# Performance work log

Hardware: AMD Instinct MI355X
Metric: run time of the kernel (lower is better)

## Reference

```python
import math
import jax, jax.numpy as jnp
import numpy as np

EPS = 1e-08
W_BLK = 256  # covers max window w = exp(log 255) + 1 = 256


def _l2norm(x):
    n = jnp.linalg.norm(x, axis=-1, keepdims=True)
    return x / jnp.maximum(n, EPS)


def setup_inputs() -> dict:
    key = jax.random.key(0)
    ks = jax.random.split(key, 7)
    B, T, Dm, H = 2, 4096, 1024, 16
    scale = 1.0 / math.sqrt(Dm)
    return {
        "query": jax.random.normal(ks[0], (B, T, Dm), jnp.float32),
        "key": jax.random.normal(ks[1], (B, T, Dm), jnp.float32),
        "value": jax.random.normal(ks[2], (B, T, Dm), jnp.float32),
        "Wq": jax.random.normal(ks[3], (Dm, Dm), jnp.float32) * scale,
        "Wk": jax.random.normal(ks[4], (Dm, Dm), jnp.float32) * scale,
        "Wv": jax.random.normal(ks[5], (Dm, Dm), jnp.float32) * scale,
        "Wo": jax.random.normal(ks[6], (Dm, Dm), jnp.float32) * scale,
        "s_v": jnp.linspace(0.0, math.log(255.0), H).astype(jnp.float32),
        "s_r": jnp.zeros((H,), jnp.float32),
    }


def _screening_forward(query, key, value, Wq, Wk, Wv, Wo, s_v, s_r):
    B, T, Dm = query.shape
    H = s_v.shape[0]
    D = Dm // H

    def proj(x, Wm):  # nn.Linear (no bias): x @ W^T, then split heads -> [B,H,T,D]
        return (x @ Wm.T).reshape(B, T, H, D).transpose(0, 2, 1, 3)

    q = _l2norm(proj(query, Wq))
    k = _l2norm(proj(key, Wk))
    v = _l2norm(proj(value, Wv))

    w = jnp.exp(s_v) + 1.0  # [H] window widths, <= 256
    r = jnp.exp(s_r) + 1.0  # [H] screening sharpness

    Wb = W_BLK
    nb = T // Wb
    qb = q.reshape(B, H, nb, Wb, D)
    kb = k.reshape(B, H, nb, Wb, D)
    vb = v.reshape(B, H, nb, Wb, D)
    # each query block attends to its own block + previous block (window <= Wb)
    kprev = jnp.pad(kb, ((0, 0), (0, 0), (1, 0), (0, 0), (0, 0)))[:, :, :nb]
    vprev = jnp.pad(vb, ((0, 0), (0, 0), (1, 0), (0, 0), (0, 0)))[:, :, :nb]
    kc = jnp.concatenate([kprev, kb], axis=3)  # [B,H,nb,2W,D]
    vc = jnp.concatenate([vprev, vb], axis=3)

    sim = jnp.einsum('bhnid,bhnjd->bhnij', qb, kc)  # [B,H,nb,W,2W]

    ii = jnp.arange(Wb)[:, None]
    jj = jnp.arange(2 * Wb)[None, :]
    rel = (jj - (Wb + ii)).astype(jnp.float32)  # [W,2W] relative offset j-i
    wb_ = w[:, None, None]  # [H,1,1]
    cos_m = 0.5 * (jnp.cos(jnp.pi * rel[None] / wb_) + 1.0)  # [H,W,2W]
    in_w = (rel[None] > -wb_) & (rel[None] <= 0.0)  # causal window
    softmask = cos_m * in_w.astype(sim.dtype)  # [H,W,2W]
    # block 0 has no previous block: first Wb key slots invalid there
    blk_valid = ((jnp.arange(nb)[:, None] > 0) | (jnp.arange(2 * Wb)[None, :] >= Wb))

    alpha = jax.nn.relu(1.0 - r[None, :, None, None, None] * (1.0 - sim)) ** 2
    alpha = alpha * softmask[None, :, None] * blk_valid.astype(sim.dtype)[None, None, :, None, :]

    out = jnp.einsum('bhnij,bhnjd->bhnid', alpha, vc).reshape(B, H, T, D)
    # TanhNorm: smoothly bound vector magnitude (tanh of the L2 norm)
    n = jnp.linalg.norm(out, axis=-1, keepdims=True)
    out = out * jnp.tanh(n) / (n + EPS)
    out = out.transpose(0, 2, 1, 3).reshape(B, T, Dm)
    return out @ Wo.T


def reference(query, key, value, Wq, Wk, Wv, Wo, s_v, s_r):
    return _screening_forward(query, key, value, Wq, Wk, Wv, Wo, s_v, s_r)
```

## Files before the change

kernel.cpp:

```cpp
#include <hip/hip_runtime.h>
#include <math.h>

#ifndef M_PI
#define M_PI 3.14159265358979323846
#endif

typedef short bf16x8 __attribute__((ext_vector_type(8)));
typedef _Float16 f16x8 __attribute__((ext_vector_type(8)));
typedef float f32x4 __attribute__((ext_vector_type(4)));

union FragU { uint4 u; bf16x8 f; };
union F16U { uint4 u; f16x8 f; _Float16 h[8]; };

typedef const __attribute__((address_space(1))) void GVoid;
typedef __attribute__((address_space(3))) void LVoid;

__device__ __forceinline__ unsigned rn_hi(float x) {
    unsigned u = __float_as_uint(x);
    unsigned r = u + 0x7FFFu + ((u >> 16) & 1u);
    return r & 0xFFFF0000u;
}

__global__ void mask_tab_kernel(const float* __restrict__ s_v, float* __restrict__ tab) {
    int h = blockIdx.x;
    int idx = threadIdx.x;
    float w = expf(s_v[h]) + 1.0f;
    float rel = (float)(idx - 255);
    float val = 0.0f;
    if (rel > -w) {
        val = 0.5f * (cosf((float)M_PI * rel / w) + 1.0f);
    }
    tab[h * 256 + idx] = val;
}

__global__ __launch_bounds__(256) void split_tiles(
        const float* __restrict__ in0, const float* __restrict__ in1,
        const float* __restrict__ in2, char* __restrict__ out0,
        unsigned long long ostride) {
    const float* in = (blockIdx.y == 0) ? in0 : (blockIdx.y == 1) ? in1 : in2;
    char* outp = out0 + (size_t)blockIdx.y * ostride;
    const int tile = blockIdx.x;
    const int kt = tile & 31;
    const int rb = tile >> 5;
    const int tid = threadIdx.x;
    const int row = tid >> 1;
    const int kc = (tid & 1) * 16;

    const float* src = in + ((size_t)(rb * 128 + row)) * 1024 + kt * 32 + kc;
    f32x4 x0 = *(const f32x4*)src;
    f32x4 x1 = *(const f32x4*)(src + 4);
    f32x4 x2 = *(const f32x4*)(src + 8);
    f32x4 x3 = *(const f32x4*)(src + 12);
    float xs[16] = {x0[0], x0[1], x0[2], x0[3], x1[0], x1[1], x1[2], x1[3],
                    x2[0], x2[1], x2[2], x2[3], x3[0], x3[1], x3[2], x3[3]};
    F16U h0, h1, l0, l1;
#pragma unroll
    for (int e = 0; e < 8; e++) {
        _Float16 h = (_Float16)xs[e];
        h0.h[e] = h;
        l0.h[e] = (_Float16)(xs[e] - (float)h);
        _Float16 h2 = (_Float16)xs[8 + e];
        h1.h[e] = h2;
        l1.h[e] = (_Float16)(xs[8 + e] - (float)h2);
    }
    char* tb = outp + (size_t)tile * 16384 + row * 128;
    const int swz = (row & 7) << 4;
    *(uint4*)(tb + ((kc * 2) ^ swz))           = h0.u;
    *(uint4*)(tb + ((kc * 2 + 16) ^ swz))      = h1.u;
    *(uint4*)(tb + ((64 + kc * 2) ^ swz))      = l0.u;
    *(uint4*)(tb + ((64 + kc * 2 + 16) ^ swz)) = l1.u;
}

__device__ __forceinline__ void cvt_split16(const f32x4* a, F16U& h0, F16U& h1,
                                            F16U& l0, F16U& l1) {
    float xs[16] = {a[0][0], a[0][1], a[0][2], a[0][3],
                    a[1][0], a[1][1], a[1][2], a[1][3],
                    a[2][0], a[2][1], a[2][2], a[2][3],
                    a[3][0], a[3][1], a[3][2], a[3][3]};
#pragma unroll
    for (int e = 0; e < 8; e++) {
        _Float16 h = (_Float16)xs[e];
        h0.h[e] = h;
        l0.h[e] = (_Float16)(xs[e] - (float)h);
        _Float16 h2 = (_Float16)xs[8 + e];
        h1.h[e] = h2;
        l1.h[e] = (_Float16)(xs[8 + e] - (float)h2);
    }
}

template <int PERM>
__global__ __launch_bounds__(256, 2) void gemm_ws(
        const float* __restrict__ A0, const float* __restrict__ A1,
        const float* __restrict__ A2,
        const char* __restrict__ Bsp, unsigned long long Bstride,
        float* __restrict__ C0, float* __restrict__ C1, float* __restrict__ C2) {
    __shared__ __align__(16) char Abuf[16384];
    __shared__ __align__(16) char Bbuf[65536];

    const int tid = threadIdx.x;
    const int bid = blockIdx.x;
    const int o = bid >> 8;
    const int x = bid & 255;
    const int xcd = x & 7;
    const int idx = x >> 3;
    const int rp = xcd * 8 + (idx >> 2);
    const int cp = idx & 3;
    const int brow = rp * 128;
    const int bcol = cp * 256;

    const float* A = (o == 0) ? A0 : (o == 1) ? A1 : A2;
    float* C = (o == 0) ? C0 : (o == 1) ? C1 : C2;
    const char* Bt = Bsp + (size_t)o * Bstride;

    const int lane = tid & 63;
    const int wid = tid >> 6;
    const int wr = wid >> 1;
    const int wc = wid & 1;
    const int l15 = lane & 15;
    const int g = lane >> 4;

    const int srow = tid >> 1;
    const int skc2 = (tid & 1) * 32;
    const float* aptr = A + (size_t)(brow + srow) * 1024 + (tid & 1) * 16;
    const int aswz = (srow & 7) << 4;
    char* awr = Abuf + srow * 128;

    const char* bsrc = Bt + ((size_t)(cp * 2 + (wid >> 1)) * 32) * 16384
                       + (wid & 1) * 8192;

    const int rswz = (l15 & 7) << 4;

    f32x4 acc[4][8];
#pragma unroll
    for (int a = 0; a < 4; a++)
#pragma unroll
        for (int b = 0; b < 8; b++) acc[a][b] = (f32x4)(0.0f);

    f32x4 areg[4];
#pragma unroll
    for (int m = 0; m < 4; m++) areg[m] = *(const f32x4*)(aptr + m * 4);
    F16U Sh0, Sh1, Sl0, Sl1;
    cvt_split16(areg, Sh0, Sh1, Sl0, Sl1);
#pragma unroll
    for (int i = 0; i < 8; i++)
        __builtin_amdgcn_global_load_lds(
            (GVoid*)(bsrc + i * 1024 + lane * 16),
            (LVoid*)(Bbuf + wid * 8192 + i * 1024), 16, 0, 0);

#pragma unroll 1
    for (int kt = 0; kt < 32; kt++) {
        __syncthreads();
        *(uint4*)(awr + ((skc2) ^ aswz))      = Sh0.u;
        *(uint4*)(awr + ((skc2 + 16) ^ aswz)) = Sh1.u;
        *(uint4*)(awr + ((skc2 + 64) ^ aswz)) = Sl0.u;
        *(uint4*)(awr + ((skc2 + 80) ^ aswz)) = Sl1.u;
        __syncthreads();

        if (kt + 1 < 32) {
            const char* bs = bsrc + (size_t)(kt + 1) * 16384;
            const int nxt = ((kt + 1) & 1) * 32768;
#pragma unroll
            for (int i = 0; i < 8; i++)
                __builtin_amdgcn_global_load_lds(
                    (GVoid*)(bs + i * 1024 + lane * 16),
                    (LVoid*)(Bbuf + nxt + wid * 8192 + i * 1024), 16, 0, 0);
#pragma unroll
            for (int m = 0; m < 4; m++)
                areg[m] = *(const f32x4*)(aptr + (kt + 1) * 32 + m * 4);
        }

        const char* bb = Bbuf + (kt & 1) * 32768 + wc * 16384;
        f16x8 ah[4], al[4];
#pragma unroll
        for (int fr = 0; fr < 4; fr++) {
            const int ro = (wr * 64 + fr * 16 + l15) * 128;
            ah[fr] = *(const f16x8*)(Abuf + ro + ((g * 16) ^ rswz));
            al[fr] = *(const f16x8*)(Abuf + ro + ((g * 16) ^ rswz ^ 64));
        }
#pragma unroll
        for (int fc = 0; fc < 8; fc++) {
            const int ro = (fc * 16 + l15) * 128;
            f16x8 bh = *(const f16x8*)(bb + ro + ((g * 16) ^ rswz));
            f16x8 bl = *(const f16x8*)(bb + ro + ((g * 16) ^ rswz ^ 64));
#pragma unroll
            for (int fr = 0; fr < 4; fr++) {
                acc[fr][fc] = __builtin_amdgcn_mfma_f32_16x16x32_f16(
                    ah[fr], bh, acc[fr][fc], 0, 0, 0);
                acc[fr][fc] = __builtin_amdgcn_mfma_f32_16x16x32_f16(
                    ah[fr], bl, acc[fr][fc], 0, 0, 0);
                acc[fr][fc] = __builtin_amdgcn_mfma_f32_16x16x32_f16(
                    al[fr], bh, acc[fr][fc], 0, 0, 0);
            }
        }
        if (kt + 1 < 32) cvt_split16(areg, Sh0, Sh1, Sl0, Sl1);
    }

    if (PERM == 1) {
#pragma unroll
        for (int fr = 0; fr < 4; fr++) {
#pragma unroll
            for (int r = 0; r < 4; r++) {
                float p0 = 0.0f, p1 = 0.0f;
#pragma unroll
                for (int fc = 0; fc < 4; fc++) {
                    p0 = fmaf(acc[fr][fc][r], acc[fr][fc][r], p0);
                    p1 = fmaf(acc[fr][fc + 4][r], acc[fr][fc + 4][r], p1);
                }
                p0 += __shfl_xor(p0, 1);  p1 += __shfl_xor(p1, 1);
                p0 += __shfl_xor(p0, 2);  p1 += __shfl_xor(p1, 2);
                p0 += __shfl_xor(p0, 4);  p1 += __shfl_xor(p1, 4);
                p0 += __shfl_xor(p0, 8);  p1 += __shfl_xor(p1, 8);
                float i0 = 1.0f / fmaxf(sqrtf(p0), 1e-8f);
                float i1 = 1.0f / fmaxf(sqrtf(p1), 1e-8f);
#pragma unroll
                for (int fc = 0; fc < 4; fc++) {
                    acc[fr][fc][r] *= i0;
                    acc[fr][fc + 4][r] *= i1;
                }
            }
        }
    }

    const int rsub = g * 4;
#pragma unroll
    for (int fr = 0; fr < 4; fr++) {
#pragma unroll
        for (int fc = 0; fc < 8; fc++) {
            f32x4 v = acc[fr][fc];
            const int i0 = brow + wr * 64 + fr * 16 + rsub;
            const int j0 = bcol + wc * 128 + fc * 16;
            if (PERM == 0) {
#pragma unroll
                for (int r = 0; r < 4; r++)
                    C[(size_t)(i0 + r) * 1024 + j0 + l15] = v[r];
            } else {
                const int h = j0 >> 6;
                const int d = (j0 & 63) + l15;
#pragma unroll
                for (int r = 0; r < 4; r++) {
                    const int i = i0 + r;
                    const int b = i >> 12;
                    const int t2 = i & 4095;
                    C[(((size_t)(b * 16 + h) * 4096 + t2) * 64 + d)] = v[r];
                }
            }
        }
    }
}

__global__ __launch_bounds__(256, 3) void attn_kernel(
        const float* __restrict__ q, const float* __restrict__ k,
        const float* __restrict__ v, const float* __restrict__ s_v,
        const float* __restrict__ s_r, const float* __restrict__ mask_tab,
        float* __restrict__ out) {
    __shared__ unsigned short Kh[32 * 72];
    __shared__ unsigned short Kl[32 * 72];
    __shared__ unsigned short Vh[64 * 40];
    __shared__ unsigned short Vl[64 * 40];
    __shared__ unsigned int   aB[4][32 * 33];
    __shared__ float          msk[256];

    const int bx = blockIdx.x;
    const int h   = bx & 15;
    const int n   = (bx >> 4) & 15;
    const int sub = (bx >> 8) & 1;
    const int b   = bx >> 9;
    const int bh = b * 16 + h;
    const int tid = threadIdx.x;
    const int lane = tid & 63;
    const int wid = tid >> 6;
    const int l15 = lane & 15;
    const int g = lane >> 4;

    msk[tid] = mask_tab[h * 256 + tid];
    const float w = expf(s_v[h]) + 1.0f;
    const float rh = expf(s_r[h]) + 1.0f;

    const int row0 = n * 256 + sub * 128;
    const float* qbase = q + (size_t)bh * 4096 * 64;
    const float* kbase = k + (size_t)bh * 4096 * 64;
    const float* vbase = v + (size_t)bh * 4096 * 64;

    bf16x8 qh[2][2], ql[2][2];
#pragma unroll
    for (int f = 0; f < 2; f++) {
#pragma unroll
        for (int ks = 0; ks < 2; ks++) {
            const float* src = qbase + (size_t)(row0 + wid * 32 + f * 16 + l15) * 64
                               + ks * 32 + g * 8;
            f32x4 x0 = *(const f32x4*)src;
            f32x4 x1 = *(const f32x4*)(src + 4);
            float xs[8] = {x0[0], x0[1], x0[2], x0[3], x1[0], x1[1], x1[2], x1[3]};
            unsigned hb[8], lb[8];
#pragma unroll
            for (int e = 0; e < 8; e++) {
                hb[e] = rn_hi(xs[e]);
                lb[e] = rn_hi(xs[e] - __uint_as_float(hb[e]));
            }
            FragU th, tl;
            th.u = make_uint4((hb[0] >> 16) | hb[1], (hb[2] >> 16) | hb[3],
                              (hb[4] >> 16) | hb[5], (hb[6] >> 16) | hb[7]);
            tl.u = make_uint4((lb[0] >> 16) | lb[1], (lb[2] >> 16) | lb[3],
                              (lb[4] >> 16) | lb[5], (lb[6] >> 16) | lb[7]);
            qh[f][ks] = th.f;
            ql[f][ks] = tl.f;
        }
    }

    int jlo = (int)floorf(256.0f + (float)(sub * 128) - w) + 1;
    if (jlo < 0) jlo = 0;
    if (n == 0 && jlo < 256) jlo = 256;
    jlo &= ~31;
    const int jhi = 256 + sub * 128 + 127;

    const int iw0 = sub * 128 + wid * 32;

    f32x4 acc[2][4];
#pragma unroll
    for (int a = 0; a < 2; a++)
#pragma unroll
        for (int d = 0; d < 4; d++) acc[a][d] = (f32x4)(0.0f);

    const int kj = tid >> 3;
    const int kd = (tid & 7) * 8;
    const int vj = tid & 31;
    const int vd = (tid >> 5) * 8;

    f32x4 kr0, kr1, vr0, vr1;
    {
        const float* ks = kbase + (size_t)((n - 1) * 256 + jlo + kj) * 64 + kd;
        const float* vs = vbase + (size_t)((n - 1) * 256 + jlo + vj) * 64 + vd;
        kr0 = *(const f32x4*)ks;  kr1 = *(const f32x4*)(ks + 4);
        vr0 = *(const f32x4*)vs;  vr1 = *(const f32x4*)(vs + 4);
    }

    for (int jt = jlo; jt <= jhi; jt += 32) {
        __syncthreads();
        {
            float xs[8] = {kr0[0], kr0[1], kr0[2], kr0[3], kr1[0], kr1[1], kr1[2], kr1[3]};
            unsigned hb[8], lb[8];
#pragma unroll
            for (int e = 0; e < 8; e++) {
                hb[e] = rn_hi(xs[e]);
                lb[e] = rn_hi(xs[e] - __uint_as_float(hb[e]));
            }
            *(uint4*)&Kh[kj * 72 + kd] =
                make_uint4((hb[0] >> 16) | hb[1], (hb[2] >> 16) | hb[3],
                           (hb[4] >> 16) | hb[5], (hb[6] >> 16) | hb[7]);
            *(uint4*)&Kl[kj * 72 + kd] =
                make_uint4((lb[0] >> 16) | lb[1], (lb[2] >> 16) | lb[3],
                           (lb[4] >> 16) | lb[5], (lb[6] >> 16) | lb[7]);
        }
        {
            float xs[8] = {vr0[0], vr0[1], vr0[2], vr0[3], vr1[0], vr1[1], vr1[2], vr1[3]};
#pragma unroll
            for (int e = 0; e < 8; e++) {
                unsigned hbv = rn_hi(xs[e]);
                unsigned lbv = rn_hi(xs[e] - __uint_as_float(hbv));
                Vh[(vd + e) * 40 + vj] = (unsigned short)(hbv >> 16);
                Vl[(vd + e) * 40 + vj] = (unsigned short)(lbv >> 16);
            }
        }
        if (jt + 32 <= jhi) {
            const float* ks = kbase + (size_t)((n - 1) * 256 + jt + 32 + kj) * 64 + kd;
            const float* vs = vbase + (size_t)((n - 1) * 256 + jt + 32 + vj) * 64 + vd;
            kr0 = *(const f32x4*)ks;  kr1 = *(const f32x4*)(ks + 4);
            vr0 = *(const f32x4*)vs;  vr1 = *(const f32x4*)(vs + 4);
        }
        __syncthreads();

        const bool live = ((float)(jt + 31) > 256.0f + (float)iw0 - w) &&
                          (jt <= 256 + iw0 + 31);
        if (live) {
            f32x4 sim[2][2];
#pragma unroll
            for (int jf = 0; jf < 2; jf++)
#pragma unroll
                for (int f = 0; f < 2; f++) sim[jf][f] = (f32x4)(0.0f);

#pragma unroll
            for (int jf = 0; jf < 2; jf++) {
#pragma unroll
                for (int ks = 0; ks < 2; ks++) {
                    bf16x8 kah = *(const bf16x8*)&Kh[(jf * 16 + l15) * 72 + ks * 32 + g * 8];
                    bf16x8 kal = *(const bf16x8*)&Kl[(jf * 16 + l15) * 72 + ks * 32 + g * 8];
#pragma unroll
                    for (int f = 0; f < 2; f++) {
                        sim[jf][f] = __builtin_amdgcn_mfma_f32_16x16x32_bf16(
                            kah, qh[f][ks], sim[jf][f], 0, 0, 0);
                        sim[jf][f] = __builtin_amdgcn_mfma_f32_16x16x32_bf16(
                            kah, ql[f][ks], sim[jf][f], 0, 0, 0);
                        sim[jf][f] = __builtin_amdgcn_mfma_f32_16x16x32_bf16(
                            kal, qh[f][ks], sim[jf][f], 0, 0, 0);
                    }
                }
            }

#pragma unroll
            for (int jf = 0; jf < 2; jf++) {
#pragma unroll
                for (int f = 0; f < 2; f++) {
#pragma unroll
                    for (int r = 0; r < 4; r++) {
                        const int jloc = jf * 16 + g * 4 + r;
                        const int iloc = f * 16 + l15;
                        const int relv = (jt + jloc) - 256 - (sub * 128 + wid * 32 + iloc);
                        float m = (relv >= -255 && relv <= 0) ? msk[relv + 255] : 0.0f;
                        float t1 = 1.0f - rh * (1.0f - sim[jf][f][r]);
                        t1 = fmaxf(t1, 0.0f);
                        float alpha = t1 * t1 * m;
                        unsigned ahb = rn_hi(alpha);
                        unsigned alb = rn_hi(alpha - __uint_as_float(ahb));
                        aB[wid][jloc * 33 + iloc] = ahb | (alb >> 16);
                    }
                }
            }

#pragma unroll
            for (int f = 0; f < 2; f++) {
                unsigned a8[8];
#pragma unroll
                for (int e = 0; e < 8; e++)
                    a8[e] = aB[wid][(g * 8 + e) * 33 + f * 16 + l15];
                FragU th, tl;
                th.u = make_uint4((a8[0] >> 16) | (a8[1] & 0xFFFF0000u),
                                  (a8[2] >> 16) | (a8[3] & 0xFFFF0000u),
                                  (a8[4] >> 16) | (a8[5] & 0xFFFF0000u),
                                  (a8[6] >> 16) | (a8[7] & 0xFFFF0000u));
                tl.u = make_uint4((a8[0] << 16 >> 16) | (a8[1] << 16),
                                  (a8[2] << 16 >> 16) | (a8[3] << 16),
                                  (a8[4] << 16 >> 16) | (a8[5] << 16),
                                  (a8[6] << 16 >> 16) | (a8[7] << 16));
                bf16x8 aah = th.f, aal = tl.f;
#pragma unroll
                for (int df = 0; df < 4; df++) {
                    bf16x8 vbh = *(const bf16x8*)&Vh[(df * 16 + l15) * 40 + g * 8];
                    bf16x8 vbl = *(const bf16x8*)&Vl[(df * 16 + l15) * 40 + g * 8];
                    acc[f][df] = __builtin_amdgcn_mfma_f32_16x16x32_bf16(
                        aah, vbh, acc[f][df], 0, 0, 0);
                    acc[f][df] = __builtin_amdgcn_mfma_f32_16x16x32_bf16(
                        aah, vbl, acc[f][df], 0, 0, 0);
                    acc[f][df] = __builtin_amdgcn_mfma_f32_16x16x32_bf16(
                        aal, vbh, acc[f][df], 0, 0, 0);
                }
            }
        }
    }

#pragma unroll
    for (int f = 0; f < 2; f++) {
#pragma unroll
        for (int r = 0; r < 4; r++) {
            float p = 0.0f;
#pragma unroll
            for (int df = 0; df < 4; df++) p = fmaf(acc[f][df][r], acc[f][df][r], p);
            p += __shfl_xor(p, 1);
            p += __shfl_xor(p, 2);
            p += __shfl_xor(p, 4);
            p += __shfl_xor(p, 8);
            float nn = sqrtf(p);
            float sc = tanhf(nn) / (nn + 1e-8f);
            const int trow = row0 + wid * 32 + f * 16 + g * 4 + r;
            float* dst = out + ((size_t)(b * 4096 + trow)) * 1024 + h * 64;
#pragma unroll
            for (int df = 0; df < 4; df++)
                dst[df * 16 + l15] = acc[f][df][r] * sc;
        }
    }
}

extern "C" void kernel_launch(void* const* d_in, const int* in_sizes, int n_in,
                              void* d_out, int out_size, void* d_ws, size_t ws_size,
                              hipStream_t stream) {
    const float* query = (const float*)d_in[0];
    const float* key   = (const float*)d_in[1];
    const float* value = (const float*)d_in[2];
    const float* Wq    = (const float*)d_in[3];
    const float* Wk    = (const float*)d_in[4];
    const float* Wv    = (const float*)d_in[5];
    const float* Wo    = (const float*)d_in[6];
    const float* s_v   = (const float*)d_in[7];
    const float* s_r   = (const float*)d_in[8];
    float* out = (float*)d_out;

    const size_t MB = 1ull << 20;
    char* base = (char*)d_ws;
    float* qw   = (float*)(base);
    float* kw   = (float*)(base + 32 * MB);
    float* vw   = (float*)(base + 64 * MB);
    float* ao   = (float*)(base + 96 * MB);
    char*  w3sp = base + 96 * MB;
    char*  wosp = base;
    float* mask = (float*)(base + 128 * MB);

    mask_tab_kernel<<<dim3(16), dim3(256), 0, stream>>>(s_v, mask);

    split_tiles<<<dim3(256, 3), dim3(256), 0, stream>>>(Wq, Wk, Wv, w3sp, 4 * MB);

    gemm_ws<1><<<dim3(768), dim3(256), 0, stream>>>(
        query, key, value, w3sp, 4 * MB, qw, kw, vw);

    attn_kernel<<<dim3(1024), dim3(256), 0, stream>>>(
        qw, kw, vw, s_v, s_r, mask, ao);

    split_tiles<<<dim3(256, 1), dim3(256), 0, stream>>>(Wo, Wo, Wo, wosp, 0);

    gemm_ws<0><<<dim3(256), dim3(256), 0, stream>>>(
        ao, ao, ao, wosp, 0, out, out, out);
}
```

Baseline: 328.9 us.

## Load A fragments directly to registers and use narrower tiles for output GEMM

```diff
diff --git a/kernel.cpp b/kernel.cpp
--- a/kernel.cpp
+++ b/kernel.cpp
@@ -71,42 +71,27 @@
     *(uint4*)(tb + ((64 + kc * 2 + 16) ^ swz)) = l1.u;
 }
 
-__device__ __forceinline__ void cvt_split16(const f32x4* a, F16U& h0, F16U& h1,
-                                            F16U& l0, F16U& l1) {
-    float xs[16] = {a[0][0], a[0][1], a[0][2], a[0][3],
-                    a[1][0], a[1][1], a[1][2], a[1][3],
-                    a[2][0], a[2][1], a[2][2], a[2][3],
-                    a[3][0], a[3][1], a[3][2], a[3][3]};
-#pragma unroll
-    for (int e = 0; e < 8; e++) {
-        _Float16 h = (_Float16)xs[e];
-        h0.h[e] = h;
-        l0.h[e] = (_Float16)(xs[e] - (float)h);
-        _Float16 h2 = (_Float16)xs[8 + e];
-        h1.h[e] = h2;
-        l1.h[e] = (_Float16)(xs[8 + e] - (float)h2);
-    }
-}
-
-template <int PERM>
-__global__ __launch_bounds__(256, 2) void gemm_ws(
+template <int PERM, int NC>
+__global__ __launch_bounds__(256, 2) void gemm_d(
         const float* __restrict__ A0, const float* __restrict__ A1,
         const float* __restrict__ A2,
         const char* __restrict__ Bsp, unsigned long long Bstride,
         float* __restrict__ C0, float* __restrict__ C1, float* __restrict__ C2) {
-    __shared__ __align__(16) char Abuf[16384];
-    __shared__ __align__(16) char Bbuf[65536];
+    constexpr int FC = NC / 32;
+    constexpr int TB = NC * 128;
+    constexpr int LPT = TB / 4096;
+    __shared__ __align__(16) char Bbuf[2 * TB];
 
     const int tid = threadIdx.x;
     const int bid = blockIdx.x;
-    const int o = bid >> 8;
-    const int x = bid & 255;
+    const int o = (NC == 256) ? (bid >> 8) : 0;
+    const int x = bid & ((NC == 256) ? 255 : 511);
     const int xcd = x & 7;
     const int idx = x >> 3;
-    const int rp = xcd * 8 + (idx >> 2);
-    const int cp = idx & 3;
+    const int rp = (NC == 256) ? (xcd * 8 + (idx >> 2)) : (xcd * 8 + (idx >> 3));
+    const int cp = (NC == 256) ? (idx & 3) : (idx & 7);
     const int brow = rp * 128;
-    const int bcol = cp * 256;
+    const int bcol = cp * NC;
 
     const float* A = (o == 0) ? A0 : (o == 1) ? A1 : A2;
     float* C = (o == 0) ? C0 : (o == 1) ? C1 : C2;
@@ -119,83 +104,99 @@
     const int l15 = lane & 15;
     const int g = lane >> 4;
 
-    const int srow = tid >> 1;
-    const int skc2 = (tid & 1) * 32;
-    const float* aptr = A + (size_t)(brow + srow) * 1024 + (tid & 1) * 16;
-    const int aswz = (srow & 7) << 4;
-    char* awr = Abuf + srow * 128;
-
-    const char* bsrc = Bt + ((size_t)(cp * 2 + (wid >> 1)) * 32) * 16384
-                       + (wid & 1) * 8192;
+    const float* aptr = A + (size_t)(brow + wr * 64 + l15) * 1024 + g * 8;
+
+    const char* bsrc = (NC == 256)
+        ? Bt + ((size_t)(cp * 2 + (wid >> 1)) * 32) * 16384 + (wid & 1) * 8192
+        : Bt + ((size_t)cp * 32) * 16384 + wid * 4096;
+    const int ldst = wid * (TB / 4);
 
     const int rswz = (l15 & 7) << 4;
 
-    f32x4 acc[4][8];
+    f32x4 acc[4][FC];
 #pragma unroll
     for (int a = 0; a < 4; a++)
 #pragma unroll
-        for (int b = 0; b < 8; b++) acc[a][b] = (f32x4)(0.0f);
-
-    f32x4 areg[4];
-#pragma unroll
-    for (int m = 0; m < 4; m++) areg[m] = *(const f32x4*)(aptr + m * 4);
-    F16U Sh0, Sh1, Sl0, Sl1;
-    cvt_split16(areg, Sh0, Sh1, Sl0, Sl1);
-#pragma unroll
-    for (int i = 0; i < 8; i++)
-        __builtin_amdgcn_global_load_lds(
-            (GVoid*)(bsrc + i * 1024 + lane * 16),
-            (LVoid*)(Bbuf + wid * 8192 + i * 1024), 16, 0, 0);
+        for (int b = 0; b < FC; b++) acc[a][b] = (f32x4)(0.0f);
+
+    f32x4 aN[4][2];
+    f16x8 ah[4], al[4];
+
+#define ISSUE_B(KT, WB)                                                        \
+    do {                                                                       \
+        const char* bs_ = bsrc + (size_t)(KT) * 16384;                         \
+        _Pragma("unroll") for (int i = 0; i < LPT; i++)                        \
+            __builtin_amdgcn_global_load_lds(                                  \
+                (GVoid*)(bs_ + i * 1024 + lane * 16),                          \
+                (LVoid*)(Bbuf + (WB) * TB + ldst + i * 1024), 16, 0, 0);       \
+    } while (0)
+
+#define ISSUE_A(KA)                                                            \
+    do {                                                                       \
+        _Pragma("unroll") for (int fr = 0; fr < 4; fr++) {                     \
+            aN[fr][0] = *(const f32x4*)(aptr + fr * 16384 + (KA) * 32);        \
+            aN[fr][1] = *(const f32x4*)(aptr + fr * 16384 + (KA) * 32 + 4);    \
+        }                                                                      \
+    } while (0)
+
+#define CVT()                                                                  \
+    do {                                                                       \
+        _Pragma("unroll") for (int fr = 0; fr < 4; fr++) {                     \
+            float xs_[8] = {aN[fr][0][0], aN[fr][0][1], aN[fr][0][2],          \
+                            aN[fr][0][3], aN[fr][1][0], aN[fr][1][1],          \
+                            aN[fr][1][2], aN[fr][1][3]};                       \
+            F16U H_, L_;                                                       \
+            _Pragma("unroll") for (int e = 0; e < 8; e++) {                    \
+                _Float16 h_ = (_Float16)xs_[e];                                \
+                H_.h[e] = h_;                                                  \
+                L_.h[e] = (_Float16)(xs_[e] - (float)h_);                      \
+            }                                                                  \
+            ah[fr] = H_.f;                                                     \
+            al[fr] = L_.f;                                                     \
+        }                                                                      \
+    } while (0)
+
+#define COMPUTE(RB)                                                            \
+    do {                                                                       \
+        const char* bb_ = Bbuf + (RB) * TB + ((NC == 256) ? wc * 16384 : 0);   \
+        _Pragma("unroll") for (int fc = 0; fc < FC; fc++) {                    \
+            const int ro_ = (((NC == 256) ? 0 : wc * 64) + fc * 16 + l15) * 128;\
+            f16x8 bh_ = *(const f16x8*)(bb_ + ro_ + ((g * 16) ^ rswz));        \
+            f16x8 bl_ = *(const f16x8*)(bb_ + ro_ + ((g * 16) ^ rswz ^ 64));   \
+            _Pragma("unroll") for (int fr = 0; fr < 4; fr++) {                 \
+                acc[fr][fc] = __builtin_amdgcn_mfma_f32_16x16x32_f16(          \
+                    ah[fr], bh_, acc[fr][fc], 0, 0, 0);                        \
+                acc[fr][fc] = __builtin_amdgcn_mfma_f32_16x16x32_f16(          \
+                    ah[fr], bl_, acc[fr][fc], 0, 0, 0);                        \
+                acc[fr][fc] = __builtin_amdgcn_mfma_f32_16x16x32_f16(          \
+                    al[fr], bh_, acc[fr][fc], 0, 0, 0);                        \
+            }                                                                  \
+        }                                                                      \
+    } while (0)
+
+    ISSUE_B(0, 0);
+    ISSUE_A(0);
+    CVT();
+    __syncthreads();
 
 #pragma unroll 1
-    for (int kt = 0; kt < 32; kt++) {
+    for (int kt = 0; kt < 32; kt += 2) {
+        if (kt + 1 < 32) { ISSUE_B(kt + 1, 1); ISSUE_A(kt + 1); }
+        COMPUTE(0);
+        if (kt + 1 < 32) CVT();
         __syncthreads();
-        *(uint4*)(awr + ((skc2) ^ aswz))      = Sh0.u;
-        *(uint4*)(awr + ((skc2 + 16) ^ aswz)) = Sh1.u;
-        *(uint4*)(awr + ((skc2 + 64) ^ aswz)) = Sl0.u;
-        *(uint4*)(awr + ((skc2 + 80) ^ aswz)) = Sl1.u;
+        if (kt + 2 < 32) { ISSUE_B(kt + 2, 0); ISSUE_A(kt + 2); }
+        COMPUTE(1);
+        if (kt + 2 < 32) CVT();
         __syncthreads();
-
-        if (kt + 1 < 32) {
-            const char* bs = bsrc + (size_t)(kt + 1) * 16384;
-            const int nxt = ((kt + 1) & 1) * 32768;
-#pragma unroll
-            for (int i = 0; i < 8; i++)
-                __builtin_amdgcn_global_load_lds(
-                    (GVoid*)(bs + i * 1024 + lane * 16),
-                    (LVoid*)(Bbuf + nxt + wid * 8192 + i * 1024), 16, 0, 0);
-#pragma unroll
-            for (int m = 0; m < 4; m++)
-                areg[m] = *(const f32x4*)(aptr + (kt + 1) * 32 + m * 4);
-        }
-
-        const char* bb = Bbuf + (kt & 1) * 32768 + wc * 16384;
-        f16x8 ah[4], al[4];
-#pragma unroll
-        for (int fr = 0; fr < 4; fr++) {
-            const int ro = (wr * 64 + fr * 16 + l15) * 128;
-            ah[fr] = *(const f16x8*)(Abuf + ro + ((g * 16) ^ rswz));
-            al[fr] = *(const f16x8*)(Abuf + ro + ((g * 16) ^ rswz ^ 64));
-        }
-#pragma unroll
-        for (int fc = 0; fc < 8; fc++) {
-            const int ro = (fc * 16 + l15) * 128;
-            f16x8 bh = *(const f16x8*)(bb + ro + ((g * 16) ^ rswz));
-            f16x8 bl = *(const f16x8*)(bb + ro + ((g * 16) ^ rswz ^ 64));
-#pragma unroll
-            for (int fr = 0; fr < 4; fr++) {
-                acc[fr][fc] = __builtin_amdgcn_mfma_f32_16x16x32_f16(
-                    ah[fr], bh, acc[fr][fc], 0, 0, 0);
-                acc[fr][fc] = __builtin_amdgcn_mfma_f32_16x16x32_f16(
-                    ah[fr], bl, acc[fr][fc], 0, 0, 0);
-                acc[fr][fc] = __builtin_amdgcn_mfma_f32_16x16x32_f16(
-                    al[fr], bh, acc[fr][fc], 0, 0, 0);
-            }
-        }
-        if (kt + 1 < 32) cvt_split16(areg, Sh0, Sh1, Sl0, Sl1);
-    }
-
-    if (PERM == 1) {
+    }
+
+#undef COMPUTE
+#undef CVT
+#undef ISSUE_A
+#undef ISSUE_B
+
+    if (PERM == 1 && NC == 256) {
 #pragma unroll
         for (int fr = 0; fr < 4; fr++) {
 #pragma unroll
@@ -221,14 +222,13 @@
         }
     }
 
-    const int rsub = g * 4;
 #pragma unroll
     for (int fr = 0; fr < 4; fr++) {
 #pragma unroll
-        for (int fc = 0; fc < 8; fc++) {
+        for (int fc = 0; fc < FC; fc++) {
             f32x4 v = acc[fr][fc];
-            const int i0 = brow + wr * 64 + fr * 16 + rsub;
-            const int j0 = bcol + wc * 128 + fc * 16;
+            const int i0 = brow + wr * 64 + fr * 16 + g * 4;
+            const int j0 = bcol + wc * (NC / 2) + fc * 16;
             if (PERM == 0) {
 #pragma unroll
                 for (int r = 0; r < 4; r++)
@@ -497,7 +497,7 @@
 
     split_tiles<<<dim3(256, 3), dim3(256), 0, stream>>>(Wq, Wk, Wv, w3sp, 4 * MB);
 
-    gemm_ws<1><<<dim3(768), dim3(256), 0, stream>>>(
+    gemm_d<1, 256><<<dim3(768), dim3(256), 0, stream>>>(
         query, key, value, w3sp, 4 * MB, qw, kw, vw);
 
     attn_kernel<<<dim3(1024), dim3(256), 0, stream>>>(
@@ -505,6 +505,6 @@
 
     split_tiles<<<dim3(256, 1), dim3(256), 0, stream>>>(Wo, Wo, Wo, wosp, 0);
 
-    gemm_ws<0><<<dim3(256), dim3(256), 0, stream>>>(
+    gemm_d<0, 128><<<dim3(512), dim3(256), 0, stream>>>(
         ao, ao, ao, wosp, 0, out, out, out);
 }
```

Result: slower. 354.0 us (+7.6%).

## Double attention rows per block and add a dedicated 128x128 output-projection GEMM

Applied to the files above, without the earlier changes.

```diff
diff --git a/kernel.cpp b/kernel.cpp
--- a/kernel.cpp
+++ b/kernel.cpp
@@ -221,13 +221,12 @@
         }
     }
 
-    const int rsub = g * 4;
 #pragma unroll
     for (int fr = 0; fr < 4; fr++) {
 #pragma unroll
         for (int fc = 0; fc < 8; fc++) {
             f32x4 v = acc[fr][fc];
-            const int i0 = brow + wr * 64 + fr * 16 + rsub;
+            const int i0 = brow + wr * 64 + fr * 16 + g * 4;
             const int j0 = bcol + wc * 128 + fc * 16;
             if (PERM == 0) {
 #pragma unroll
@@ -248,7 +247,133 @@
     }
 }
 
-__global__ __launch_bounds__(256, 3) void attn_kernel(
+__global__ __launch_bounds__(256, 2) void gemm_wo(
+        const float* __restrict__ A0,
+        const char* __restrict__ Bsp,
+        float* __restrict__ C0) {
+    constexpr int FC = 4;
+    constexpr int TB = 16384;
+    __shared__ __align__(16) char Bbuf[2 * TB];
+
+    const int tid = threadIdx.x;
+    const int x = blockIdx.x & 511;
+    const int xcd = x & 7;
+    const int idx = x >> 3;
+    const int rp = xcd * 8 + (idx >> 3);
+    const int cp = idx & 7;
+    const int brow = rp * 128;
+    const int bcol = cp * 128;
+
+    const int lane = tid & 63;
+    const int wid = tid >> 6;
+    const int wr = wid >> 1;
+    const int wc = wid & 1;
+    const int l15 = lane & 15;
+    const int g = lane >> 4;
+
+    const float* aptr = A0 + (size_t)(brow + wr * 64 + l15) * 1024 + g * 8;
+    const char* bsrc = Bsp + ((size_t)cp * 32) * 16384 + wid * 4096;
+    const int ldst = wid * (TB / 4);
+    const int rswz = (l15 & 7) << 4;
+
+    f32x4 acc[4][FC];
+#pragma unroll
+    for (int a = 0; a < 4; a++)
+#pragma unroll
+        for (int b = 0; b < FC; b++) acc[a][b] = (f32x4)(0.0f);
+
+    f32x4 aN[4][2];
+    f16x8 ah[4], al[4];
+
+#define ISSUE_B(KT, WB)                                                        \
+    do {                                                                       \
+        const char* bs_ = bsrc + (size_t)(KT) * 16384;                         \
+        _Pragma("unroll") for (int i = 0; i < 4; i++)                          \
+            __builtin_amdgcn_global_load_lds(                                  \
+                (GVoid*)(bs_ + i * 1024 + lane * 16),                          \
+                (LVoid*)(Bbuf + (WB) * TB + ldst + i * 1024), 16, 0, 0);       \
+    } while (0)
+
+#define ISSUE_A(KA)                                                            \
+    do {                                                                       \
+        _Pragma("unroll") for (int fr = 0; fr < 4; fr++) {                     \
+            aN[fr][0] = *(const f32x4*)(aptr + fr * 16384 + (KA) * 32);        \
+            aN[fr][1] = *(const f32x4*)(aptr + fr * 16384 + (KA) * 32 + 4);    \
+        }                                                                      \
+    } while (0)
+
+#define CVT()                                                                  \
+    do {                                                                       \
+        _Pragma("unroll") for (int fr = 0; fr < 4; fr++) {                     \
+            float xs_[8] = {aN[fr][0][0], aN[fr][0][1], aN[fr][0][2],          \
+                            aN[fr][0][3], aN[fr][1][0], aN[fr][1][1],          \
+                            aN[fr][1][2], aN[fr][1][3]};                       \
+            F16U H_, L_;                                                       \
+            _Pragma("unroll") for (int e = 0; e < 8; e++) {                    \
+                _Float16 h_ = (_Float16)xs_[e];                                \
+                H_.h[e] = h_;                                                  \
+                L_.h[e] = (_Float16)(xs_[e] - (float)h_);                      \
+            }                                                                  \
+            ah[fr] = H_.f;                                                     \
+            al[fr] = L_.f;                                                     \
+        }                                                                      \
+    } while (0)
+
+#define COMPUTE(RB)                                                            \
+    do {                                                                       \
+        const char* bb_ = Bbuf + (RB) * TB;                                    \
+        _Pragma("unroll") for (int fc = 0; fc < FC; fc++) {                    \
+            const int ro_ = (wc * 64 + fc * 16 + l15) * 128;                   \
+            f16x8 bh_ = *(const f16x8*)(bb_ + ro_ + ((g * 16) ^ rswz));        \
+            f16x8 bl_ = *(const f16x8*)(bb_ + ro_ + ((g * 16) ^ rswz ^ 64));   \
+            _Pragma("unroll") for (int fr = 0; fr < 4; fr++) {                 \
+                acc[fr][fc] = __builtin_amdgcn_mfma_f32_16x16x32_f16(          \
+                    ah[fr], bh_, acc[fr][fc], 0, 0, 0);                        \
+                acc[fr][fc] = __builtin_amdgcn_mfma_f32_16x16x32_f16(          \
+                    ah[fr], bl_, acc[fr][fc], 0, 0, 0);                        \
+                acc[fr][fc] = __builtin_amdgcn_mfma_f32_16x16x32_f16(          \
+                    al[fr], bh_, acc[fr][fc], 0, 0, 0);                        \
+            }                                                                  \
+        }                                                                      \
+    } while (0)
+
+    ISSUE_B(0, 0);
+    ISSUE_A(0);
+    CVT();
+    __syncthreads();
+
+#pragma unroll 1
+    for (int kt = 0; kt < 32; kt += 2) {
+        if (kt + 1 < 32) { ISSUE_B(kt + 1, 1); ISSUE_A(kt + 1); }
+        COMPUTE(0);
+        if (kt + 1 < 32) CVT();
+        __syncthreads();
+        if (kt + 2 < 32) { ISSUE_B(kt + 2, 0); ISSUE_A(kt + 2); }
+        COMPUTE(1);
+        if (kt + 2 < 32) CVT();
+        __syncthreads();
+    }
+
+#undef COMPUTE
+#undef CVT
+#undef ISSUE_A
+#undef ISSUE_B
+
+#pragma unroll
+    for (int fr = 0; fr < 4; fr++) {
+#pragma unroll
+        for (int fc = 0; fc < FC; fc++) {
+            f32x4 v = acc[fr][fc];
+            const int i0 = brow + wr * 64 + fr * 16 + g * 4;
+            const int j0 = bcol + wc * 64 + fc * 16;
+#pragma unroll
+            for (int r = 0; r < 4; r++)
+                C0[(size_t)(i0 + r) * 1024 + j0 + l15] = v[r];
+        }
+    }
+}
+
+__global__ __launch_bounds__(256, 2) void attn_kernel(
         const float* __restrict__ q, const float* __restrict__ k,
         const float* __restrict__ v, const float* __restrict__ s_v,
         const float* __restrict__ s_r, const float* __restrict__ mask_tab,
@@ -257,14 +382,13 @@
     __shared__ unsigned short Kl[32 * 72];
     __shared__ unsigned short Vh[64 * 40];
     __shared__ unsigned short Vl[64 * 40];
-    __shared__ unsigned int   aB[4][32 * 33];
+    __shared__ unsigned int   aB[4][32 * 65];
     __shared__ float          msk[256];
 
     const int bx = blockIdx.x;
-    const int h   = bx & 15;
-    const int n   = (bx >> 4) & 15;
-    const int sub = (bx >> 8) & 1;
-    const int b   = bx >> 9;
+    const int h = bx & 15;
+    const int n = (bx >> 4) & 15;
+    const int b = bx >> 8;
     const int bh = b * 16 + h;
     const int tid = threadIdx.x;
     const int lane = tid & 63;
@@ -276,17 +400,17 @@
     const float w = expf(s_v[h]) + 1.0f;
     const float rh = expf(s_r[h]) + 1.0f;
 
-    const int row0 = n * 256 + sub * 128;
+    const int row0 = n * 256;
     const float* qbase = q + (size_t)bh * 4096 * 64;
     const float* kbase = k + (size_t)bh * 4096 * 64;
     const float* vbase = v + (size_t)bh * 4096 * 64;
 
-    bf16x8 qh[2][2], ql[2][2];
-#pragma unroll
-    for (int f = 0; f < 2; f++) {
+    bf16x8 qh[4][2], ql[4][2];
+#pragma unroll
+    for (int f = 0; f < 4; f++) {
 #pragma unroll
         for (int ks = 0; ks < 2; ks++) {
-            const float* src = qbase + (size_t)(row0 + wid * 32 + f * 16 + l15) * 64
+            const float* src = qbase + (size_t)(row0 + wid * 64 + f * 16 + l15) * 64
                                + ks * 32 + g * 8;
             f32x4 x0 = *(const f32x4*)src;
             f32x4 x1 = *(const f32x4*)(src + 4);
@@ -307,17 +431,17 @@
         }
     }
 
-    int jlo = (int)floorf(256.0f + (float)(sub * 128) - w) + 1;
+    int jlo = (int)floorf(256.0f - w) + 1;
     if (jlo < 0) jlo = 0;
     if (n == 0 && jlo < 256) jlo = 256;
     jlo &= ~31;
-    const int jhi = 256 + sub * 128 + 127;
-
-    const int iw0 = sub * 128 + wid * 32;
-
-    f32x4 acc[2][4];
-#pragma unroll
-    for (int a = 0; a < 2; a++)
+    const int jhi = 511;
+
+    const int iw0 = wid * 64;
+
+    f32x4 acc[4][4];
+#pragma unroll
+    for (int a = 0; a < 4; a++)
 #pragma unroll
         for (int d = 0; d < 4; d++) acc[a][d] = (f32x4)(0.0f);
 
@@ -370,13 +494,13 @@
         __syncthreads();
 
         const bool live = ((float)(jt + 31) > 256.0f + (float)iw0 - w) &&
-                          (jt <= 256 + iw0 + 31);
+                          (jt <= 256 + iw0 + 63);
         if (live) {
-            f32x4 sim[2][2];
+            f32x4 sim[2][4];
 #pragma unroll
             for (int jf = 0; jf < 2; jf++)
 #pragma unroll
-                for (int f = 0; f < 2; f++) sim[jf][f] = (f32x4)(0.0f);
+                for (int f = 0; f < 4; f++) sim[jf][f] = (f32x4)(0.0f);
 
 #pragma unroll
             for (int jf = 0; jf < 2; jf++) {
@@ -385,7 +509,7 @@
                     bf16x8 kah = *(const bf16x8*)&Kh[(jf * 16 + l15) * 72 + ks * 32 + g * 8];
                     bf16x8 kal = *(const bf16x8*)&Kl[(jf * 16 + l15) * 72 + ks * 32 + g * 8];
 #pragma unroll
-                    for (int f = 0; f < 2; f++) {
+                    for (int f = 0; f < 4; f++) {
                         sim[jf][f] = __builtin_amdgcn_mfma_f32_16x16x32_bf16(
                             kah, qh[f][ks], sim[jf][f], 0, 0, 0);
                         sim[jf][f] = __builtin_amdgcn_mfma_f32_16x16x32_bf16(
@@ -399,29 +523,29 @@
 #pragma unroll
             for (int jf = 0; jf < 2; jf++) {
 #pragma unroll
-                for (int f = 0; f < 2; f++) {
+                for (int f = 0; f < 4; f++) {
 #pragma unroll
                     for (int r = 0; r < 4; r++) {
                         const int jloc = jf * 16 + g * 4 + r;
                         const int iloc = f * 16 + l15;
-                        const int relv = (jt + jloc) - 256 - (sub * 128 + wid * 32 + iloc);
+                        const int relv = (jt + jloc) - 256 - (iw0 + iloc);
                         float m = (relv >= -255 && relv <= 0) ? msk[relv + 255] : 0.0f;
                         float t1 = 1.0f - rh * (1.0f - sim[jf][f][r]);
                         t1 = fmaxf(t1, 0.0f);
                         float alpha = t1 * t1 * m;
                         unsigned ahb = rn_hi(alpha);
                         unsigned alb = rn_hi(alpha - __uint_as_float(ahb));
-                        aB[wid][jloc * 33 + iloc] = ahb | (alb >> 16);
+                        aB[wid][jloc * 65 + iloc] = ahb | (alb >> 16);
                     }
                 }
             }
 
 #pragma unroll
-            for (int f = 0; f < 2; f++) {
+            for (int f = 0; f < 4; f++) {
                 unsigned a8[8];
 #pragma unroll
                 for (int e = 0; e < 8; e++)
-                    a8[e] = aB[wid][(g * 8 + e) * 33 + f * 16 + l15];
+                    a8[e] = aB[wid][(g * 8 + e) * 65 + f * 16 + l15];
                 FragU th, tl;
                 th.u = make_uint4((a8[0] >> 16) | (a8[1] & 0xFFFF0000u),
                                   (a8[2] >> 16) | (a8[3] & 0xFFFF0000u),
@@ -448,7 +572,7 @@
     }
 
 #pragma unroll
-    for (int f = 0; f < 2; f++) {
+    for (int f = 0; f < 4; f++) {
 #pragma unroll
         for (int r = 0; r < 4; r++) {
             float p = 0.0f;
@@ -460,7 +584,7 @@
             p += __shfl_xor(p, 8);
             float nn = sqrtf(p);
             float sc = tanhf(nn) / (nn + 1e-8f);
-            const int trow = row0 + wid * 32 + f * 16 + g * 4 + r;
+            const int trow = row0 + wid * 64 + f * 16 + g * 4 + r;
             float* dst = out + ((size_t)(b * 4096 + trow)) * 1024 + h * 64;
 #pragma unroll
             for (int df = 0; df < 4; df++)
@@ -500,11 +624,10 @@
     gemm_ws<1><<<dim3(768), dim3(256), 0, stream>>>(
         query, key, value, w3sp, 4 * MB, qw, kw, vw);
 
-    attn_kernel<<<dim3(1024), dim3(256), 0, stream>>>(
+    attn_kernel<<<dim3(512), dim3(256), 0, stream>>>(
         qw, kw, vw, s_v, s_r, mask, ao);
 
     split_tiles<<<dim3(256, 1), dim3(256), 0, stream>>>(Wo, Wo, Wo, wosp, 0);
 
-    gemm_ws<0><<<dim3(256), dim3(256), 0, stream>>>(
-        ao, ao, ao, wosp, 0, out, out, out);
-}
+    gemm_wo<<<dim3(512), dim3(256), 0, stream>>>(ao, wosp, out);
+}
```

Measured after the change: 338.5 us. +2.9%, slower.
